# Performance work log

Measured on AMD Instinct MI355X. Metric: run time of the kernel, lower is better.

## Reference

```python
import jax, jax.numpy as jnp
import numpy as np

NUM_CLASSES = 20
MIN_CLASS_SIZE = 5000
EPS = 1e-6

B, C, H, W = 2, 64, 384, 384


def setup_inputs() -> dict:
    key = jax.random.key(0)
    k1, k2, k3 = jax.random.split(key, 3)
    hyperspectral_image = jax.random.normal(k1, (B, C, H, W), dtype=jnp.float32)
    methane_pattern = jax.random.normal(k2, (C,), dtype=jnp.float32)
    segmentation_mask = jax.random.randint(k3, (B, H, W), 0, NUM_CLASSES, dtype=jnp.int32)
    return {
        "hyperspectral_image": hyperspectral_image,
        "methane_pattern": methane_pattern,
        "segmentation_mask": segmentation_mask,
    }


def reference(hyperspectral_image, methane_pattern, segmentation_mask):
    b, c, h, w = hyperspectral_image.shape
    n = h * w
    # pixels: (B, N, C); seg: (B, N)
    x = jnp.transpose(hyperspectral_image, (0, 2, 3, 1)).reshape(b, n, c)
    seg = segmentation_mask.reshape(b, n)
    onehot = jax.nn.one_hot(seg, NUM_CLASSES, dtype=x.dtype)  # (B, N, K)

    counts = onehot.sum(axis=1)                                # (B, K)
    safe_counts = jnp.maximum(counts, 1.0)
    sums = jnp.einsum('bnk,bnc->bkc', onehot, x)               # (B, K, C)
    mean = sums / safe_counts[..., None]                       # (B, K, C)

    # Second moment per class: X_k^T X_k, then cov = E[xx^T] - mu mu^T + eps*I
    sxx = jnp.einsum('bnk,bnc,bnd->bkcd', onehot, x, x)        # (B, K, C, C)
    cov = sxx / safe_counts[..., None, None] - jnp.einsum('bkc,bkd->bkcd', mean, mean)
    cov = cov + EPS * jnp.eye(c, dtype=x.dtype)
    inv_cov = jnp.linalg.inv(cov)                              # (B, K, C, C)

    p = methane_pattern
    w_filt = jnp.einsum('bkcd,d->bkc', inv_cov, p)             # Sigma^-1 p, (B, K, C)
    denom = jnp.sqrt(jnp.einsum('c,bkc->bk', p, w_filt))       # (B, K)

    valid = (counts >= MIN_CLASS_SIZE).astype(x.dtype)         # (B, K)

    # Gather per-pixel class stats via one-hot (exact partition)
    mean_px = jnp.einsum('bnk,bkc->bnc', onehot, mean)         # (B, N, C)
    w_px = jnp.einsum('bnk,bkc->bnc', onehot, w_filt)          # (B, N, C)
    denom_px = jnp.einsum('bnk,bk->bn', onehot, denom)         # (B, N)
    valid_px = jnp.einsum('bnk,bk->bn', onehot, valid)         # (B, N)

    score = jnp.sum((x - mean_px) * w_px, axis=-1) / denom_px  # (B, N)
    score = score * valid_px
    return score.reshape(b, h, w)
```

## Files before the change

kernel.cpp:

```cpp
#include <hip/hip_runtime.h>
#include <math.h>

#define NCLS 20
#define CH 64
#define NPIX (384*384)
#define BATCH 2
#define MINSZ 5000
#define EPSV 1e-6f
#define NCHUNK 16
#define NBLK (BATCH*NPIX/256)
#define BLKPERB (NPIX/256)
#define PSTRIDE 4160
#define CAP 8192
#define XSTR 72
#define ROWOFF(c) ((c)*XSTR + ((c)>>3)*8)
#define TSTR 260

typedef __attribute__((ext_vector_type(8))) __bf16 bf16x8;
typedef __attribute__((ext_vector_type(4))) float  f32x4;

static __device__ inline unsigned short f2bf(float f) {
    unsigned u = __builtin_bit_cast(unsigned, f);
    return (unsigned short)((u + 0x7fffu + ((u >> 16) & 1u)) >> 16);
}
static __device__ inline float bf2f(unsigned us) {
    unsigned u = us << 16;
    return __builtin_bit_cast(float, u);
}

__global__ void __launch_bounds__(256) k_hist(const int* __restrict__ seg, int* __restrict__ hist) {
    __shared__ int wcnt[4][NCLS];
    int t = threadIdx.x, blk = blockIdx.x;
    int wave = t >> 6, lane = t & 63;
    int k = seg[blk * 256 + t];
    #pragma unroll
    for (int cls = 0; cls < NCLS; ++cls) {
        unsigned long long m = __ballot(k == cls);
        if (lane == 0) wcnt[wave][cls] = __popcll(m);
    }
    __syncthreads();
    if (t < NCLS)
        hist[t * NBLK + blk] = wcnt[0][t] + wcnt[1][t] + wcnt[2][t] + wcnt[3][t];
}

__global__ void __launch_bounds__(256) k_scanall(const int* __restrict__ hist,
        int* __restrict__ counts, int* __restrict__ blockbase) {
    int bk = blockIdx.x;
    int b = bk / NCLS, k = bk % NCLS;
    int t = threadIdx.x;
    __shared__ int sh[BLKPERB];
    __shared__ int tpA[256], tpB[256];

    const int* hb = hist + (size_t)k * NBLK + b * BLKPERB;
    for (int e = t; e < BLKPERB; e += 256) sh[e] = hb[e];
    __syncthreads();

    int s0 = 0, s1 = 0, s2 = 0;
    if (t < 192) {
        s0 = sh[3*t];
        s1 = s0 + sh[3*t + 1];
        s2 = s1 + sh[3*t + 2];
    }
    int mytot = (t < 192) ? s2 : 0;
    tpA[t] = mytot;
    __syncthreads();
    tpB[t] = tpA[t] + ((t >= 1)   ? tpA[t-1]   : 0); __syncthreads();
    tpA[t] = tpB[t] + ((t >= 2)   ? tpB[t-2]   : 0); __syncthreads();
    tpB[t] = tpA[t] + ((t >= 4)   ? tpA[t-4]   : 0); __syncthreads();
    tpA[t] = tpB[t] + ((t >= 8)   ? tpB[t-8]   : 0); __syncthreads();
    tpB[t] = tpA[t] + ((t >= 16)  ? tpA[t-16]  : 0); __syncthreads();
    tpA[t] = tpB[t] + ((t >= 32)  ? tpB[t-32]  : 0); __syncthreads();
    tpB[t] = tpA[t] + ((t >= 64)  ? tpA[t-64]  : 0); __syncthreads();
    tpA[t] = tpB[t] + ((t >= 128) ? tpB[t-128] : 0); __syncthreads();

    if (t == 191) counts[bk] = tpA[191];
    if (t < 192) {
        int excl = bk * CAP + tpA[t] - mytot;
        int* bb = blockbase + ((size_t)b * BLKPERB) * NCLS + k;
        bb[(3*t    ) * NCLS] = excl;
        bb[(3*t + 1) * NCLS] = excl + s0;
        bb[(3*t + 2) * NCLS] = excl + s1;
    }
}

__global__ void __launch_bounds__(256) k_scatter(const float* __restrict__ x, const int* __restrict__ seg,
                          const int* __restrict__ blockbase, unsigned short* __restrict__ gathered,
                          int* __restrict__ rowsrc) {
    __shared__ __align__(16) float tile2[32 * TSTR];
    __shared__ int wcnt[4][NCLS];
    __shared__ int sblk[NCLS];
    __shared__ int drow[256];
    __shared__ int sinv[256];
    int t = threadIdx.x;
    int blk = blockIdx.x;
    int base = blk * 256;
    int b = base / NPIX;
    int k = seg[base + t];
    int wave = t >> 6, lane = t & 63;

    int riw = 0;
    for (int cls = 0; cls < NCLS; ++cls) {
        unsigned long long m = __ballot(k == cls);
        if (lane == 0) wcnt[wave][cls] = __popcll(m);
        if (k == cls) riw = __popcll(m & ((1ull << lane) - 1ull));
    }
    __syncthreads();
    if (t < NCLS) {
        int s = 0;
        for (int c = 0; c < t; ++c) s += wcnt[0][c] + wcnt[1][c] + wcnt[2][c] + wcnt[3][c];
        sblk[t] = s;
    }
    __syncthreads();
    int rib = riw;
    for (int w = 0; w < 4; ++w) if (w < wave) rib += wcnt[w][k];
    int slot = sblk[k] + rib;
    int myrow = blockbase[blk * NCLS + k] + rib;
    drow[slot] = myrow;
    sinv[slot] = t;
    rowsrc[myrow] = base + t;
    const float* xc = x + (size_t)b * CH * NPIX + (base - b * NPIX);

    for (int ph = 0; ph < 2; ++ph) {
        __syncthreads();
        #pragma unroll
        for (int i = 0; i < 8; ++i) {
            int cc = i * 4 + wave;
            float4 xv = *(const float4*)(xc + (size_t)(ph * 32 + cc) * NPIX + 4 * lane);
            *(float4*)(tile2 + cc * TSTR + 4 * lane) = xv;
        }
        __syncthreads();
        #pragma unroll
        for (int it = 0; it < 16; ++it) {
            int f = it * 256 + t;
            int s = f >> 4, c2 = f & 15;
            int r = sinv[s];
            float lo = tile2[(2 * c2    ) * TSTR + r];
            float hi = tile2[(2 * c2 + 1) * TSTR + r];
            unsigned pk = (unsigned)f2bf(lo) | ((unsigned)f2bf(hi) << 16);
            *(unsigned*)(gathered + (size_t)drow[s] * CH + ph * 32 + 2 * c2) = pk;
        }
    }
}

__global__ void __launch_bounds__(256) k_gemm(const unsigned short* __restrict__ gathered,
        const int* __restrict__ counts, float* __restrict__ partials) {
    __shared__ __align__(16) unsigned short xt[64 * XSTR + 7 * 8];
    __shared__ float wsum[4][CH];
    int id = blockIdx.x;
    int chunk = id % NCHUNK;
    int bk = id / NCHUNK;
    int cnt = counts[bk];
    int off = bk * CAP;
    int csz = (cnt + NCHUNK - 1) / NCHUNK;
    int p0 = chunk * csz;
    int pend = min(cnt, p0 + csz);
    int t = threadIdx.x;
    int w = t >> 6, l = t & 63, g = l >> 4, c15 = l & 15;
    int cg = t & 7;
    int ppair = t >> 3;

    f32x4 acc[4];
    #pragma unroll
    for (int nb = 0; nb < 4; ++nb) { f32x4 z = {0.f,0.f,0.f,0.f}; acc[nb] = z; }
    float ssum[8] = {0.f,0.f,0.f,0.f,0.f,0.f,0.f,0.f};

    for (int tp = p0; tp < pend; tp += 64) {
        __syncthreads();
        {
            int gp0 = tp + 2 * ppair, gp1 = gp0 + 1;
            uint4 v0 = make_uint4(0u,0u,0u,0u), v1 = make_uint4(0u,0u,0u,0u);
            if (gp0 < pend) v0 = *(const uint4*)(gathered + (size_t)(off + gp0) * CH + cg * 8);
            if (gp1 < pend) v1 = *(const uint4*)(gathered + (size_t)(off + gp1) * CH + cg * 8);
            unsigned a0[4] = {v0.x, v0.y, v0.z, v0.w};
            unsigned a1[4] = {v1.x, v1.y, v1.z, v1.w};
            #pragma unroll
            for (int q = 0; q < 4; ++q) {
                unsigned lo0 = a0[q] & 0xffffu, hi0 = a0[q] >> 16;
                unsigned lo1 = a1[q] & 0xffffu, hi1 = a1[q] >> 16;
                ssum[2*q]   += bf2f(lo0) + bf2f(lo1);
                ssum[2*q+1] += bf2f(hi0) + bf2f(hi1);
                int ch0 = 8 * cg + 2 * q;
                *(unsigned*)(xt + ROWOFF(ch0)     + 2 * ppair) = lo0 | (lo1 << 16);
                *(unsigned*)(xt + ROWOFF(ch0 + 1) + 2 * ppair) = hi0 | (hi1 << 16);
            }
        }
        __syncthreads();
        #pragma unroll
        for (int kc = 0; kc < 2; ++kc) {
            bf16x8 fr0 = *(const bf16x8*)(xt + ROWOFF( 0 + c15) + kc * 32 + 8 * g);
            bf16x8 fr1 = *(const bf16x8*)(xt + ROWOFF(16 + c15) + kc * 32 + 8 * g);
            bf16x8 fr2 = *(const bf16x8*)(xt + ROWOFF(32 + c15) + kc * 32 + 8 * g);
            bf16x8 fr3 = *(const bf16x8*)(xt + ROWOFF(48 + c15) + kc * 32 + 8 * g);
            bf16x8 fa;
            if      (w == 0) fa = fr0;
            else if (w == 1) fa = fr1;
            else if (w == 2) fa = fr2;
            else             fa = fr3;
            acc[0] = __builtin_amdgcn_mfma_f32_16x16x32_bf16(fa, fr0, acc[0], 0, 0, 0);
            acc[1] = __builtin_amdgcn_mfma_f32_16x16x32_bf16(fa, fr1, acc[1], 0, 0, 0);
            acc[2] = __builtin_amdgcn_mfma_f32_16x16x32_bf16(fa, fr2, acc[2], 0, 0, 0);
            acc[3] = __builtin_amdgcn_mfma_f32_16x16x32_bf16(fa, fr3, acc[3], 0, 0, 0);
        }
    }

    float* pout = partials + (size_t)id * PSTRIDE;
    #pragma unroll
    for (int nb = 0; nb < 4; ++nb)
        #pragma unroll
        for (int r = 0; r < 4; ++r)
            pout[(16*w + 4*g + r) * 64 + 16*nb + c15] = acc[nb][r];

    #pragma unroll
    for (int o = 8; o < 64; o <<= 1)
        #pragma unroll
        for (int j = 0; j < 8; ++j) ssum[j] += __shfl_xor(ssum[j], o);
    if (l < 8) {
        #pragma unroll
        for (int j = 0; j < 8; ++j) wsum[w][l * 8 + j] = ssum[j];
    }
    __syncthreads();
    if (t < CH) pout[4096 + t] = wsum[0][t] + wsum[1][t] + wsum[2][t] + wsum[3][t];
}

__global__ void __launch_bounds__(256) k_reduce(const float* __restrict__ partials,
        float* __restrict__ sxxred) {
    int id = blockIdx.x;
    int bk = id / 17, slice = id % 17;
    int t = threadIdx.x;
    const float* pp = partials + (size_t)bk * NCHUNK * PSTRIDE;
    if (slice < 16) {
        int e = slice * 256 + t;
        float v = 0.f;
        #pragma unroll
        for (int ch = 0; ch < NCHUNK; ++ch) v += pp[(size_t)ch * PSTRIDE + e];
        sxxred[(size_t)bk * PSTRIDE + e] = v;
    } else if (t < CH) {
        float v = 0.f;
        #pragma unroll
        for (int ch = 0; ch < NCHUNK; ++ch) v += pp[(size_t)ch * PSTRIDE + 4096 + t];
        sxxred[(size_t)bk * PSTRIDE + 4096 + t] = v;
    }
}

__global__ void __launch_bounds__(64) k_solve(const float* __restrict__ sxxred,
        const int* __restrict__ counts, const float* __restrict__ pattern,
        float* __restrict__ params) {
    int bk = blockIdx.x;
    int lane = threadIdx.x;
    __shared__ __align__(16) float sA[64];
    __shared__ __align__(16) float sB[64];
    __shared__ float smean[64];
    __shared__ __align__(16) float sT[64 * 65];

    const float* pp = sxxred + (size_t)bk * PSTRIDE;
    int cnt = counts[bk];
    float inv = 1.0f / fmaxf((float)cnt, 1.0f);
    float mean_own = pp[4096 + lane] * inv;
    float pat_own = pattern[lane];
    float rhs_own = pat_own;
    smean[lane] = mean_own;
    __syncthreads();

    float Mc[64];
    #pragma unroll
    for (int r = 0; r < 64; ++r) {
        float s = pp[r * 64 + lane];
        float cov = s * inv - smean[r] * mean_own;
        Mc[r] = cov + ((r == lane) ? EPSV : 0.f);
    }

    float pinv_own = 0.f;
    #pragma unroll
    for (int J = 0; J < 64; J += 2) {
        sA[lane] = Mc[J];
        sB[lane] = Mc[J + 1];
        __syncthreads();
        float pinvA = 1.0f / sA[J];
        float aJ1   = sA[J + 1];
        float fJ1   = aJ1 * pinvA;
        float pivB  = sB[J + 1] - fJ1 * aJ1;
        float pinvB = 1.0f / pivB;
        if (lane == J)     pinv_own = pinvA;
        if (lane == J + 1) pinv_own = pinvB;
        float McJ  = Mc[J];
        float McJ1 = fmaf(-fJ1, McJ, Mc[J + 1]);
        Mc[J + 1] = McJ1;
        float rA = __shfl(rhs_own, J);
        if (lane > J) rhs_own = fmaf(-McJ * pinvA, rA, rhs_own);
        float rB = __shfl(rhs_own, J + 1);
        if (lane > J + 1) rhs_own = fmaf(-McJ1 * pinvB, rB, rhs_own);
        #pragma unroll
        for (int i = (J + 2) >> 2; i < 16; ++i) {
            float4 av = *((const float4*)sA + i);
            float4 bv = *((const float4*)sB + i);
            float avq[4] = {av.x, av.y, av.z, av.w};
            float bvq[4] = {bv.x, bv.y, bv.z, bv.w};
            #pragma unroll
            for (int q = 0; q < 4; ++q) {
                int r = 4 * i + q;
                if (r > J + 1) {
                    float fA = avq[q] * pinvA;
                    float m1 = fmaf(-fA, aJ1, bvq[q]);
                    float fB = m1 * pinvB;
                    float v = fmaf(-fA, McJ, Mc[r]);
                    Mc[r] = fmaf(-fB, McJ1, v);
                }
            }
        }
        __syncthreads();
    }

    #pragma unroll
    for (int r = 0; r < 64; ++r) sT[lane * 65 + r] = Mc[r];
    __syncthreads();

    #pragma unroll
    for (int gq = 0; gq < 8; ++gq) {
        float u[8];
        #pragma unroll
        for (int m = 0; m < 8; ++m)
            u[m] = sT[(63 - (gq * 8 + m)) * 65 + lane];
        #pragma unroll
        for (int m = 0; m < 8; ++m) {
            int j = 63 - (gq * 8 + m);
            float wj = __shfl(rhs_own * pinv_own, j);
            if (lane < j) rhs_own = fmaf(-u[m], wj, rhs_own);
        }
    }
    float w_own = rhs_own * pinv_own;

    float dp = pat_own * w_own;
    float bias = mean_own * w_own;
    #pragma unroll
    for (int o = 32; o > 0; o >>= 1) {
        dp += __shfl_xor(dp, o);
        bias += __shfl_xor(bias, o);
    }
    float denom = sqrtf(dp);
    float valid = (cnt >= MINSZ) ? 1.0f : 0.0f;
    float scale = (denom > 0.f) ? (valid / denom) : 0.0f;
    params[bk * 66 + lane] = w_own * scale;
    if (lane == 0) {
        params[bk * 66 + 64] = bias * scale;
        params[bk * 66 + 65] = 0.f;
    }
}

__global__ void __launch_bounds__(256) k_score(const unsigned short* __restrict__ gathered,
        const int* __restrict__ rowsrc, const int* __restrict__ counts,
        const float* __restrict__ params, float* __restrict__ out) {
    int id = blockIdx.x;
    int bk = id >> 5, sub = id & 31;
    int cnt = counts[bk];
    int row0 = sub * 256;
    if (row0 >= cnt) return;
    int t = threadIdx.x;
    int wave = t >> 6, l = t & 63, lg = l & 7;

    float wc[8];
    #pragma unroll
    for (int j = 0; j < 8; ++j) wc[j] = params[bk * 66 + lg * 8 + j];
    float bias = params[bk * 66 + 64];

    #pragma unroll
    for (int it = 0; it < 8; ++it) {
        int rloc = row0 + it * 32 + wave * 8 + (l >> 3);
        if (rloc < cnt) {
            uint4 v = *(const uint4*)(gathered + (size_t)(bk * CAP + rloc) * CH + lg * 8);
            unsigned arr[4] = {v.x, v.y, v.z, v.w};
            float dot = 0.f;
            #pragma unroll
            for (int q = 0; q < 4; ++q) {
                dot = fmaf(bf2f(arr[q] & 0xffffu), wc[2*q],   dot);
                dot = fmaf(bf2f(arr[q] >> 16),     wc[2*q+1], dot);
            }
            dot += __shfl_xor(dot, 1);
            dot += __shfl_xor(dot, 2);
            dot += __shfl_xor(dot, 4);
            if (lg == 0)
                out[rowsrc[bk * CAP + rloc]] = dot - bias;
        }
    }
}

extern "C" void kernel_launch(void* const* d_in, const int* in_sizes, int n_in,
                              void* d_out, int out_size, void* d_ws, size_t ws_size,
                              hipStream_t stream) {
    const float* x       = (const float*)d_in[0];
    const float* pattern = (const float*)d_in[1];
    const int*   seg     = (const int*)d_in[2];
    float* out = (float*)d_out;

    unsigned short* gathered = (unsigned short*)d_ws;
    float* partials = (float*)(gathered + (size_t)BATCH * NCLS * CAP * CH);
    float* sxxred   = partials + (size_t)BATCH * NCLS * NCHUNK * PSTRIDE;
    float* params   = sxxred + (size_t)BATCH * NCLS * PSTRIDE;
    int* hist       = (int*)(params + BATCH * NCLS * 66);
    int* blockbase  = hist + NCLS * NBLK;
    int* counts     = blockbase + NBLK * NCLS;
    int* rowsrc     = counts + BATCH * NCLS;

    k_hist   <<<NBLK,               256, 0, stream>>>(seg, hist);
    k_scanall<<<BATCH*NCLS,         256, 0, stream>>>(hist, counts, blockbase);
    k_scatter<<<NBLK,               256, 0, stream>>>(x, seg, blockbase, gathered, rowsrc);
    k_gemm   <<<BATCH*NCLS*NCHUNK,  256, 0, stream>>>(gathered, counts, partials);
    k_reduce <<<BATCH*NCLS*17,      256, 0, stream>>>(partials, sxxred);
    k_solve  <<<BATCH*NCLS,          64, 0, stream>>>(sxxred, counts, pattern, params);
    k_score  <<<BATCH*NCLS*(CAP/256), 256, 0, stream>>>(gathered, rowsrc, counts, params, out);
}
```

Baseline: 98.40 us.

## Fuse partial reduction into gemm via last-block atomic semaphore; pad transpose stride

Removes the separate k_reduce launch. Each gemm block bumps a per-class atomic counter, and the last block to finish for a class sums the sixteen partials into sxxred. A memset is added to zero the semaphores each call. The shared transpose tile stride also changes from 260 to 261 to reduce LDS bank conflicts in the scatter gather. The trade-off is a serialized reduction tail in one block per class, plus an extra memset launch.

```diff
diff --git a/kernel.cpp b/kernel.cpp
--- a/kernel.cpp
+++ b/kernel.cpp
@@ -14,7 +14,7 @@
 #define CAP 8192
 #define XSTR 72
 #define ROWOFF(c) ((c)*XSTR + ((c)>>3)*8)
-#define TSTR 260
+#define TSTR 261
 
 typedef __attribute__((ext_vector_type(8))) __bf16 bf16x8;
 typedef __attribute__((ext_vector_type(4))) float  f32x4;
@@ -143,9 +143,11 @@
 }
 
 __global__ void __launch_bounds__(256) k_gemm(const unsigned short* __restrict__ gathered,
-        const int* __restrict__ counts, float* __restrict__ partials) {
+        const int* __restrict__ counts, float* __restrict__ partials,
+        int* __restrict__ sem, float* __restrict__ sxxred) {
     __shared__ __align__(16) unsigned short xt[64 * XSTR + 7 * 8];
     __shared__ float wsum[4][CH];
+    __shared__ int s_last;
     int id = blockIdx.x;
     int chunk = id % NCHUNK;
     int bk = id / NCHUNK;
@@ -220,25 +222,20 @@
     }
     __syncthreads();
     if (t < CH) pout[4096 + t] = wsum[0][t] + wsum[1][t] + wsum[2][t] + wsum[3][t];
-}
-
-__global__ void __launch_bounds__(256) k_reduce(const float* __restrict__ partials,
-        float* __restrict__ sxxred) {
-    int id = blockIdx.x;
-    int bk = id / 17, slice = id % 17;
-    int t = threadIdx.x;
-    const float* pp = partials + (size_t)bk * NCHUNK * PSTRIDE;
-    if (slice < 16) {
-        int e = slice * 256 + t;
+
+    __threadfence();
+    if (t == 0) s_last = (atomicAdd(&sem[bk], 1) == NCHUNK - 1) ? 1 : 0;
+    __syncthreads();
+    if (!s_last) return;
+    __threadfence();
+
+    const float* pbase = partials + (size_t)bk * NCHUNK * PSTRIDE;
+    float* sred = sxxred + (size_t)bk * PSTRIDE;
+    for (int e = t; e < PSTRIDE; e += 256) {
         float v = 0.f;
         #pragma unroll
-        for (int ch = 0; ch < NCHUNK; ++ch) v += pp[(size_t)ch * PSTRIDE + e];
-        sxxred[(size_t)bk * PSTRIDE + e] = v;
-    } else if (t < CH) {
-        float v = 0.f;
-        #pragma unroll
-        for (int ch = 0; ch < NCHUNK; ++ch) v += pp[(size_t)ch * PSTRIDE + 4096 + t];
-        sxxred[(size_t)bk * PSTRIDE + 4096 + t] = v;
+        for (int ch = 0; ch < NCHUNK; ++ch) v += pbase[(size_t)ch * PSTRIDE + e];
+        sred[e] = v;
     }
 }
 
@@ -399,12 +396,13 @@
     int* blockbase  = hist + NCLS * NBLK;
     int* counts     = blockbase + NBLK * NCLS;
     int* rowsrc     = counts + BATCH * NCLS;
-
+    int* sem        = rowsrc + BATCH * NCLS * CAP;
+
+    hipMemsetAsync(sem, 0, BATCH * NCLS * sizeof(int), stream);
     k_hist   <<<NBLK,               256, 0, stream>>>(seg, hist);
     k_scanall<<<BATCH*NCLS,         256, 0, stream>>>(hist, counts, blockbase);
     k_scatter<<<NBLK,               256, 0, stream>>>(x, seg, blockbase, gathered, rowsrc);
-    k_gemm   <<<BATCH*NCLS*NCHUNK,  256, 0, stream>>>(gathered, counts, partials);
-    k_reduce <<<BATCH*NCLS*17,      256, 0, stream>>>(partials, sxxred);
+    k_gemm   <<<BATCH*NCLS*NCHUNK,  256, 0, stream>>>(gathered, counts, partials, sem, sxxred);
     k_solve  <<<BATCH*NCLS,          64, 0, stream>>>(sxxred, counts, pattern, params);
     k_score  <<<BATCH*NCLS*(CAP/256), 256, 0, stream>>>(gathered, rowsrc, counts, params, out);
 }
```

New measurement: 193.9 us. 1.97x slower.
